# Kernel optimization log

Hardware: AMD Instinct MI355X
Metric: run time of the kernel (lower is better)

The kernel has to match this reference:

```python
import jax, jax.numpy as jnp
import numpy as np
from jax import lax

H = 512   # hidden_size
O = 256   # output_size
B = 64    # batch
S = 1024  # encoder sequence length
T = 256   # decoder timesteps


def setup_inputs() -> dict:
    key = jax.random.key(0)
    ks = jax.random.split(key, 10)
    bound = 1.0 / np.sqrt(H)  # PyTorch LSTM/Linear init scale
    return {
        "encoder_outputs": jax.random.normal(ks[0], (B, S, H), jnp.float32),
        "hidden": jax.random.normal(ks[1], (1, B, H), jnp.float32),
        "cell": jax.random.normal(ks[2], (1, B, H), jnp.float32),
        "target": jax.random.normal(ks[3], (B, T, O), jnp.float32),
        # LSTM params (gate order i, f, g, o as in PyTorch)
        "W_ih": jax.random.uniform(ks[4], (4 * H, H + O), jnp.float32, -bound, bound),
        "W_hh": jax.random.uniform(ks[5], (4 * H, H), jnp.float32, -bound, bound),
        "b_ih": jax.random.uniform(ks[6], (4 * H,), jnp.float32, -bound, bound),
        "b_hh": jax.random.uniform(ks[7], (4 * H,), jnp.float32, -bound, bound),
        # FC params
        "W_fc": jax.random.uniform(ks[8], (O, H), jnp.float32, -bound, bound),
        "b_fc": jax.random.uniform(ks[9], (O,), jnp.float32, -bound, bound),
    }


def reference(encoder_outputs, hidden, cell, target, W_ih, W_hh, b_ih, b_hh, W_fc, b_fc):
    h0 = hidden[0]  # [B, H]
    c0 = cell[0]    # [B, H]

    def step(carry, x_t):
        h, c = carry
        # Attention: dot-product scores over encoder positions
        scores = jnp.einsum("bsh,bh->bs", encoder_outputs, h)      # [B, S]
        attn = jax.nn.softmax(scores, axis=1)
        context = jnp.einsum("bs,bsh->bh", attn, encoder_outputs)  # [B, H]
        x = jnp.concatenate([context, x_t], axis=-1)               # [B, H+O]
        # Single-step LSTM cell (PyTorch gate order i, f, g, o)
        gates = x @ W_ih.T + b_ih + h @ W_hh.T + b_hh              # [B, 4H]
        i_g, f_g, g_g, o_g = jnp.split(gates, 4, axis=-1)
        i_g = jax.nn.sigmoid(i_g)
        f_g = jax.nn.sigmoid(f_g)
        g_g = jnp.tanh(g_g)
        o_g = jax.nn.sigmoid(o_g)
        c_new = f_g * c + i_g * g_g
        h_new = o_g * jnp.tanh(c_new)
        out = h_new @ W_fc.T + b_fc                                # [B, O]
        return (h_new, c_new), out

    _, outs = lax.scan(step, (h0, c0), jnp.swapaxes(target, 0, 1))  # outs: [T, B, O]
    return jnp.swapaxes(outs, 0, 1)  # [B, T, O]
```

## Files before the change

kernel.cpp:

```cpp
#include <hip/hip_runtime.h>

#define HH 512
#define OO 256
#define BB 64
#define SS 1024
#define TT 256
#define KK 1280

typedef __attribute__((ext_vector_type(8))) short bh8;
typedef __attribute__((ext_vector_type(8))) _Float16 hf8;
typedef __attribute__((ext_vector_type(4))) float fx4;

__device__ __forceinline__ unsigned short f2bf(float x) {
    union { float f; unsigned int u; } v; v.f = x;
    unsigned int r = v.u + 0x7fffu + ((v.u >> 16) & 1u);
    return (unsigned short)(r >> 16);
}
__device__ __forceinline__ float bf2f(unsigned short s) {
    union { unsigned int u; float f; } z; z.u = ((unsigned int)s) << 16; return z.f;
}

__global__ void prep_weights(const float* __restrict__ W_ih,
                             const float* __restrict__ W_hh,
                             unsigned short* __restrict__ wfH,
                             unsigned short* __restrict__ wfL) {
    int g = blockIdx.x * 256 + threadIdx.x;
    if (g >= 64 * 40 * 2 * 64) return;
    int lane = g & 63;
    int nt = (g >> 6) & 1;
    int kk = (g >> 7) % 40;
    int ht = (g >> 7) / 40;
    int c = nt * 16 + (lane & 15);
    int gate = c >> 3, rr = c & 7;
    int j = gate * 512 + ht * 8 + rr;
    int kbase = kk * 32 + (lane >> 4) * 8;
    unsigned short* dh = wfH + (size_t)g * 8;
    unsigned short* dl = wfL + (size_t)g * 8;
#pragma unroll
    for (int r = 0; r < 8; ++r) {
        int k = kbase + r;
        float v = (k < 768) ? W_ih[(size_t)j * 768 + k]
                            : W_hh[(size_t)j * 512 + (k - 768)];
        unsigned short hi = f2bf(v);
        dh[r] = hi;
        dl[r] = f2bf(v - bf2f(hi));
    }
}

__global__ void prep_misc(const float* __restrict__ hidden,
                          const float* __restrict__ cell,
                          float* __restrict__ h, float* __restrict__ c) {
    const int total = 32768 + 32768;
    for (int i = blockIdx.x * 256 + threadIdx.x; i < total; i += gridDim.x * 256) {
        if (i < 32768) h[i] = hidden[i];
        else           c[i - 32768] = cell[i - 32768];
    }
}

__global__ void prep_enc(const float* __restrict__ enc,
                         _Float16* __restrict__ ench) {
    const size_t i = ((size_t)blockIdx.x * 256 + threadIdx.x) * 8;
    const float4 a = *(const float4*)(enc + i);
    const float4 b = *(const float4*)(enc + i + 4);
    hf8 o;
    o[0] = (_Float16)a.x; o[1] = (_Float16)a.y;
    o[2] = (_Float16)a.z; o[3] = (_Float16)a.w;
    o[4] = (_Float16)b.x; o[5] = (_Float16)b.y;
    o[6] = (_Float16)b.z; o[7] = (_Float16)b.w;
    *(hf8*)(ench + i) = o;
}

__device__ __forceinline__ void fc_unit(int v, int tprev,
                                        const float* __restrict__ h,
                                        const float* __restrict__ W_fc,
                                        const float* __restrict__ b_fc,
                                        float* __restrict__ out,
                                        float (*shacc)[64]) {
    const int tid = threadIdx.x;
    const int b = v >> 2, oq = v & 3;
    const int ol = tid & 63, kq = tid >> 6;
    const int o = oq * 64 + ol;
    float acc = 0.f;
    const float* hp = h + b * HH + kq * 128;
    const float* wp = W_fc + (size_t)o * HH + kq * 128;
#pragma unroll 8
    for (int k2 = 0; k2 < 128; ++k2) acc += hp[k2] * wp[k2];
    shacc[kq][ol] = acc;
    __syncthreads();
    if (tid < 64) {
        float vv = shacc[0][tid] + shacc[1][tid]
                 + shacc[2][tid] + shacc[3][tid] + b_fc[oq * 64 + tid];
        out[((size_t)b * TT + tprev) * OO + oq * 64 + tid] = vv;
    }
}

template <int ENCF16>
__global__ void __launch_bounds__(256)
step_attnp(int t, const float* __restrict__ enc,
           const _Float16* __restrict__ ench,
           const float* __restrict__ h,
           float* __restrict__ pm, float* __restrict__ pl,
           float* __restrict__ pctx,
           const float* __restrict__ W_fc, const float* __restrict__ b_fc,
           float* __restrict__ out) {
    const int tid = threadIdx.x;
    const int lane = tid & 63;
    const int w = tid >> 6;

    __shared__ union {
        struct { float m[4]; float l[4]; float ctx[4][512]; } a;
        struct { float acc[4][64]; } o;
    } sh;

    const int u = blockIdx.x;
    if (u < 1024) {
        const int b = u >> 4, ch = u & 15;
        float m = -3.0e38f, l = 0.f;
        if (ENCF16) {
            const float* hb = h + b * HH + lane * 8;
            const float4 h0 = *(const float4*)hb;
            const float4 h1 = *(const float4*)(hb + 4);
            float cx[8];
#pragma unroll
            for (int j = 0; j < 8; ++j) cx[j] = 0.f;
            const _Float16* er =
                ench + ((size_t)(b * SS + ch * 64 + w * 16)) * HH + lane * 8;
            for (int rp = 0; rp < 8; ++rp) {
                const hf8 ev = *(const hf8*)er;
                const hf8 fv = *(const hf8*)(er + HH);
                float e[8], f[8];
#pragma unroll
                for (int j = 0; j < 8; ++j) {
                    e[j] = (float)ev[j];
                    f[j] = (float)fv[j];
                }
                float dA = e[0]*h0.x + e[1]*h0.y + e[2]*h0.z + e[3]*h0.w
                         + e[4]*h1.x + e[5]*h1.y + e[6]*h1.z + e[7]*h1.w;
                float dB = f[0]*h0.x + f[1]*h0.y + f[2]*h0.z + f[3]*h0.w
                         + f[4]*h1.x + f[5]*h1.y + f[6]*h1.z + f[7]*h1.w;
#pragma unroll
                for (int off = 32; off; off >>= 1) {
                    dA += __shfl_xor(dA, off);
                    dB += __shfl_xor(dB, off);
                }
                const float mx = fmaxf(dA, dB);
                if (mx > m) {
                    const float fs = __expf(m - mx);
                    l *= fs;
#pragma unroll
                    for (int j = 0; j < 8; ++j) cx[j] *= fs;
                    m = mx;
                }
                const float pA = __expf(dA - m);
                const float pB = __expf(dB - m);
                l += pA + pB;
#pragma unroll
                for (int j = 0; j < 8; ++j) cx[j] += pA * e[j] + pB * f[j];
                er += 2 * HH;
            }
            if (lane == 0) { sh.a.m[w] = m; sh.a.l[w] = l; }
            *(float4*)&sh.a.ctx[w][lane * 8]     = make_float4(cx[0], cx[1], cx[2], cx[3]);
            *(float4*)&sh.a.ctx[w][lane * 8 + 4] = make_float4(cx[4], cx[5], cx[6], cx[7]);
        } else {
            const float4 h0 = *(const float4*)(h + b * HH + lane * 4);
            const float4 h1 = *(const float4*)(h + b * HH + 256 + lane * 4);
            float4 c0 = {0, 0, 0, 0}, c1 = {0, 0, 0, 0};
            const float* er = enc + ((size_t)(b * SS + ch * 64 + w * 16)) * HH;
            for (int rp = 0; rp < 8; ++rp) {
                const float4 e0 = *(const float4*)(er + lane * 4);
                const float4 e1 = *(const float4*)(er + 256 + lane * 4);
                const float4 f0 = *(const float4*)(er + HH + lane * 4);
                const float4 f1 = *(const float4*)(er + HH + 256 + lane * 4);
                float dA = e0.x * h0.x + e0.y * h0.y + e0.z * h0.z + e0.w * h0.w
                         + e1.x * h1.x + e1.y * h1.y + e1.z * h1.z + e1.w * h1.w;
                float dB = f0.x * h0.x + f0.y * h0.y + f0.z * h0.z + f0.w * h0.w
                         + f1.x * h1.x + f1.y * h1.y + f1.z * h1.z + f1.w * h1.w;
#pragma unroll
                for (int off = 32; off; off >>= 1) {
                    dA += __shfl_xor(dA, off);
                    dB += __shfl_xor(dB, off);
                }
                const float mx = fmaxf(dA, dB);
                if (mx > m) {
                    const float fs = __expf(m - mx);
                    l *= fs;
                    c0.x *= fs; c0.y *= fs; c0.z *= fs; c0.w *= fs;
                    c1.x *= fs; c1.y *= fs; c1.z *= fs; c1.w *= fs;
                    m = mx;
                }
                const float pA = __expf(dA - m);
                const float pB = __expf(dB - m);
                l += pA + pB;
                c0.x += pA * e0.x + pB * f0.x; c0.y += pA * e0.y + pB * f0.y;
                c0.z += pA * e0.z + pB * f0.z; c0.w += pA * e0.w + pB * f0.w;
                c1.x += pA * e1.x + pB * f1.x; c1.y += pA * e1.y + pB * f1.y;
                c1.z += pA * e1.z + pB * f1.z; c1.w += pA * e1.w + pB * f1.w;
                er += 2 * HH;
            }
            if (lane == 0) { sh.a.m[w] = m; sh.a.l[w] = l; }
            *(float4*)&sh.a.ctx[w][lane * 4] = c0;
            *(float4*)&sh.a.ctx[w][256 + lane * 4] = c1;
        }
        __syncthreads();
        float M = fmaxf(fmaxf(sh.a.m[0], sh.a.m[1]), fmaxf(sh.a.m[2], sh.a.m[3]));
        float wg[4]; float ls = 0.f;
#pragma unroll
        for (int q = 0; q < 4; ++q) { wg[q] = __expf(sh.a.m[q] - M); ls += wg[q] * sh.a.l[q]; }
        const int hh = tid * 2;
        float v0 = wg[0] * sh.a.ctx[0][hh] + wg[1] * sh.a.ctx[1][hh]
                 + wg[2] * sh.a.ctx[2][hh] + wg[3] * sh.a.ctx[3][hh];
        float v1 = wg[0] * sh.a.ctx[0][hh + 1] + wg[1] * sh.a.ctx[1][hh + 1]
                 + wg[2] * sh.a.ctx[2][hh + 1] + wg[3] * sh.a.ctx[3][hh + 1];
        float* pc = pctx + ((size_t)(b * 16 + ch)) * HH;
        *(float2*)(pc + hh) = make_float2(v0, v1);
        if (tid == 0) { pm[b * 16 + ch] = M; pl[b * 16 + ch] = ls; }
    } else if (t > 0) {
        fc_unit(u - 1024, t - 1, h, W_fc, b_fc, out, sh.o.acc);
    }
}

__global__ void __launch_bounds__(256)
step_combine(int t, const float* __restrict__ target, const float* __restrict__ h,
             const float* __restrict__ pm, const float* __restrict__ pl,
             const float* __restrict__ pctx,
             unsigned short* __restrict__ xbh, unsigned short* __restrict__ xbl) {
    const int tid = threadIdx.x;
    const int b = blockIdx.x;
    float Mb = -3.0e38f;
#pragma unroll
    for (int q2 = 0; q2 < 16; ++q2) Mb = fmaxf(Mb, pm[b * 16 + q2]);
    float wq[16]; float lsb = 0.f;
#pragma unroll
    for (int q2 = 0; q2 < 16; ++q2) {
        wq[q2] = __expf(pm[b * 16 + q2] - Mb);
        lsb += wq[q2] * pl[b * 16 + q2];
    }
    const float inv = 1.0f / lsb;
    const int h2 = tid * 2;
    float s0 = 0.f, s1 = 0.f;
#pragma unroll
    for (int q2 = 0; q2 < 16; ++q2) {
        const float* pc2 = pctx + ((size_t)(b * 16 + q2)) * HH + h2;
        s0 += wq[q2] * pc2[0];
        s1 += wq[q2] * pc2[1];
    }
    s0 *= inv; s1 *= inv;
    unsigned short a0 = f2bf(s0), a1 = f2bf(s1);
    xbh[b * KK + h2]     = a0;  xbl[b * KK + h2]     = f2bf(s0 - bf2f(a0));
    xbh[b * KK + h2 + 1] = a1;  xbl[b * KK + h2 + 1] = f2bf(s1 - bf2f(a1));
    if (tid < 128) {
        const float* tg = target + ((size_t)b * TT + t) * OO + tid * 2;
        unsigned short t0 = f2bf(tg[0]), t1 = f2bf(tg[1]);
        xbh[b * KK + 512 + tid * 2]     = t0;
        xbh[b * KK + 512 + tid * 2 + 1] = t1;
        xbl[b * KK + 512 + tid * 2]     = f2bf(tg[0] - bf2f(t0));
        xbl[b * KK + 512 + tid * 2 + 1] = f2bf(tg[1] - bf2f(t1));
    }
    const float hv0 = h[b * HH + h2], hv1 = h[b * HH + h2 + 1];
    unsigned short g0 = f2bf(hv0), g1 = f2bf(hv1);
    xbh[b * KK + 768 + h2]     = g0;  xbl[b * KK + 768 + h2]     = f2bf(hv0 - bf2f(g0));
    xbh[b * KK + 768 + h2 + 1] = g1;  xbl[b * KK + 768 + h2 + 1] = f2bf(hv1 - bf2f(g1));
}

__global__ void __launch_bounds__(256)
step_gates(const unsigned short* __restrict__ xbh,
           const unsigned short* __restrict__ xbl,
           const unsigned short* __restrict__ wfH,
           const unsigned short* __restrict__ wfL,
           const float* __restrict__ b_ih, const float* __restrict__ b_hh,
           float* __restrict__ h, float* __restrict__ c) {
    const int tid = threadIdx.x;
    const int lane = tid & 63;
    const int w = tid >> 6;
    __shared__ float g[64][32];

    const int ht = blockIdx.x;
    fx4 a0 = {0, 0, 0, 0}, a1 = {0, 0, 0, 0};
    const int bro = 16 * w + (lane & 15);
    const int kg = lane >> 4;
    const size_t wbase = (size_t)ht * 40 * 2 * 512;
    for (int kk = 0; kk < 40; ++kk) {
        const size_t aoff = (size_t)bro * KK + kk * 32 + kg * 8;
        bh8 avh = *(const bh8*)(xbh + aoff);
        bh8 avl = *(const bh8*)(xbl + aoff);
        bh8 b0h = *(const bh8*)(wfH + wbase + (kk * 2 + 0) * 512 + lane * 8);
        bh8 b1h = *(const bh8*)(wfH + wbase + (kk * 2 + 1) * 512 + lane * 8);
        bh8 b0l = *(const bh8*)(wfL + wbase + (kk * 2 + 0) * 512 + lane * 8);
        bh8 b1l = *(const bh8*)(wfL + wbase + (kk * 2 + 1) * 512 + lane * 8);
        a0 = __builtin_amdgcn_mfma_f32_16x16x32_bf16(avh, b0h, a0, 0, 0, 0);
        a0 = __builtin_amdgcn_mfma_f32_16x16x32_bf16(avl, b0h, a0, 0, 0, 0);
        a0 = __builtin_amdgcn_mfma_f32_16x16x32_bf16(avh, b0l, a0, 0, 0, 0);
        a1 = __builtin_amdgcn_mfma_f32_16x16x32_bf16(avh, b1h, a1, 0, 0, 0);
        a1 = __builtin_amdgcn_mfma_f32_16x16x32_bf16(avl, b1h, a1, 0, 0, 0);
        a1 = __builtin_amdgcn_mfma_f32_16x16x32_bf16(avh, b1l, a1, 0, 0, 0);
    }
    const int crow = (lane >> 4) * 4;
#pragma unroll
    for (int r = 0; r < 4; ++r) {
        g[16 * w + crow + r][lane & 15]        = a0[r];
        g[16 * w + crow + r][16 + (lane & 15)] = a1[r];
    }
    __syncthreads();
#pragma unroll
    for (int p = 0; p < 2; ++p) {
        const int idx = tid * 2 + p;
        const int b = idx >> 3, r = idx & 7;
        const int hidx = ht * 8 + r;
        float gi = g[b][r]      + b_ih[hidx]        + b_hh[hidx];
        float gf = g[b][8 + r]  + b_ih[512 + hidx]  + b_hh[512 + hidx];
        float gg = g[b][16 + r] + b_ih[1024 + hidx] + b_hh[1024 + hidx];
        float go = g[b][24 + r] + b_ih[1536 + hidx] + b_hh[1536 + hidx];
        float ig = 1.f / (1.f + __expf(-gi));
        float fg = 1.f / (1.f + __expf(-gf));
        float g2 = tanhf(gg);
        float og = 1.f / (1.f + __expf(-go));
        float cn = fg * c[b * HH + hidx] + ig * g2;
        float hn = og * tanhf(cn);
        c[b * HH + hidx] = cn;
        h[b * HH + hidx] = hn;
    }
}

__global__ void __launch_bounds__(256)
fc_final(const float* __restrict__ h, const float* __restrict__ W_fc,
         const float* __restrict__ b_fc, float* __restrict__ out) {
    __shared__ float acc[4][64];
    fc_unit(blockIdx.x, TT - 1, h, W_fc, b_fc, out, acc);
}

extern "C" void kernel_launch(void* const* d_in, const int* in_sizes, int n_in,
                              void* d_out, int out_size, void* d_ws, size_t ws_size,
                              hipStream_t stream) {
    const float* enc    = (const float*)d_in[0];
    const float* hidden = (const float*)d_in[1];
    const float* cellp  = (const float*)d_in[2];
    const float* target = (const float*)d_in[3];
    const float* W_ih   = (const float*)d_in[4];
    const float* W_hh   = (const float*)d_in[5];
    const float* b_ih   = (const float*)d_in[6];
    const float* b_hh   = (const float*)d_in[7];
    const float* W_fc   = (const float*)d_in[8];
    const float* b_fc   = (const float*)d_in[9];
    float* out = (float*)d_out;

    char* base = (char*)d_ws;
    float* h              = (float*)(base + 0);
    float* c              = (float*)(base + 131072);
    unsigned short* wfH   = (unsigned short*)(base + 262144);
    unsigned short* wfL   = (unsigned short*)(base + 5505024);
    unsigned short* xbh   = (unsigned short*)(base + 10747904);
    unsigned short* xbl   = (unsigned short*)(base + 10911744);
    float* pm             = (float*)(base + 11075584);
    float* pl             = (float*)(base + 11079680);
    float* pctx           = (float*)(base + 11083776);
    _Float16* ench        = (_Float16*)(base + 13180928);
    const size_t NEED_H = 13180928ULL + 67108864ULL;

    const bool use_ench = (ws_size >= NEED_H);

    prep_weights<<<dim3(1280), dim3(256), 0, stream>>>(W_ih, W_hh, wfH, wfL);
    prep_misc<<<dim3(256), dim3(256), 0, stream>>>(hidden, cellp, h, c);
    if (use_ench)
        prep_enc<<<dim3(16384), dim3(256), 0, stream>>>(enc, ench);

    for (int t = 0; t < TT; ++t) {
        if (use_ench)
            step_attnp<1><<<dim3(1280), dim3(256), 0, stream>>>(
                t, enc, ench, h, pm, pl, pctx, W_fc, b_fc, out);
        else
            step_attnp<0><<<dim3(1280), dim3(256), 0, stream>>>(
                t, enc, ench, h, pm, pl, pctx, W_fc, b_fc, out);
        step_combine<<<dim3(64), dim3(256), 0, stream>>>(
            t, target, h, pm, pl, pctx, xbh, xbl);
        step_gates<<<dim3(64), dim3(256), 0, stream>>>(
            xbh, xbl, wfH, wfL, b_ih, b_hh, h, c);
    }
    fc_final<<<dim3(256), dim3(256), 0, stream>>>(h, W_fc, b_fc, out);
}
```

Measured before the change: 10.53 ms.

## Use fp16 for FC weights and partial contexts, unroll attention by four

Converts W_fc to fp16 once in the prep kernel and reads it in the per-step FC, and stores the per-chunk attention context partials as fp16 instead of fp32. The attention loop now processes four encoder rows per iteration with a single online-softmax rescale, which gives more loads in flight and fewer max/rescale branches. The fp32 encoder fallback is removed and the fp16 encoder copy is made unconditional, even though the workspace size is no longer checked. These changes cut memory traffic and instruction overhead in the recurrent loop, at the cost of lower precision in the FC weights and context partials.

```diff
diff --git a/kernel.cpp b/kernel.cpp
--- a/kernel.cpp
+++ b/kernel.cpp
@@ -10,20 +10,21 @@
 typedef __attribute__((ext_vector_type(8))) short bh8;
 typedef __attribute__((ext_vector_type(8))) _Float16 hf8;
 typedef __attribute__((ext_vector_type(4))) float fx4;
-
-__device__ __forceinline__ unsigned short f2bf(float x) {
+typedef unsigned short ushort_t;
+
+__device__ __forceinline__ ushort_t f2bf(float x) {
     union { float f; unsigned int u; } v; v.f = x;
     unsigned int r = v.u + 0x7fffu + ((v.u >> 16) & 1u);
-    return (unsigned short)(r >> 16);
-}
-__device__ __forceinline__ float bf2f(unsigned short s) {
+    return (ushort_t)(r >> 16);
+}
+__device__ __forceinline__ float bf2f(ushort_t s) {
     union { unsigned int u; float f; } z; z.u = ((unsigned int)s) << 16; return z.f;
 }
 
 __global__ void prep_weights(const float* __restrict__ W_ih,
                              const float* __restrict__ W_hh,
-                             unsigned short* __restrict__ wfH,
-                             unsigned short* __restrict__ wfL) {
+                             ushort_t* __restrict__ wfH,
+                             ushort_t* __restrict__ wfL) {
     int g = blockIdx.x * 256 + threadIdx.x;
     if (g >= 64 * 40 * 2 * 64) return;
     int lane = g & 63;
@@ -34,14 +35,14 @@
     int gate = c >> 3, rr = c & 7;
     int j = gate * 512 + ht * 8 + rr;
     int kbase = kk * 32 + (lane >> 4) * 8;
-    unsigned short* dh = wfH + (size_t)g * 8;
-    unsigned short* dl = wfL + (size_t)g * 8;
+    ushort_t* dh = wfH + (size_t)g * 8;
+    ushort_t* dl = wfL + (size_t)g * 8;
 #pragma unroll
     for (int r = 0; r < 8; ++r) {
         int k = kbase + r;
         float v = (k < 768) ? W_ih[(size_t)j * 768 + k]
                             : W_hh[(size_t)j * 512 + (k - 768)];
-        unsigned short hi = f2bf(v);
+        ushort_t hi = f2bf(v);
         dh[r] = hi;
         dl[r] = f2bf(v - bf2f(hi));
     }
@@ -49,16 +50,19 @@
 
 __global__ void prep_misc(const float* __restrict__ hidden,
                           const float* __restrict__ cell,
-                          float* __restrict__ h, float* __restrict__ c) {
-    const int total = 32768 + 32768;
+                          const float* __restrict__ W_fc,
+                          float* __restrict__ h, float* __restrict__ c,
+                          _Float16* __restrict__ wfc16) {
+    const int total = 32768 + 32768 + 131072;
     for (int i = blockIdx.x * 256 + threadIdx.x; i < total; i += gridDim.x * 256) {
-        if (i < 32768) h[i] = hidden[i];
-        else           c[i - 32768] = cell[i - 32768];
-    }
-}
-
-__global__ void prep_enc(const float* __restrict__ enc,
-                         _Float16* __restrict__ ench) {
+        if (i < 32768)       h[i] = hidden[i];
+        else if (i < 65536)  c[i - 32768] = cell[i - 32768];
+        else                 wfc16[i - 65536] = (_Float16)W_fc[i - 65536];
+    }
+}
+
+__global__ void prep_ench(const float* __restrict__ enc,
+                          _Float16* __restrict__ ench) {
     const size_t i = ((size_t)blockIdx.x * 256 + threadIdx.x) * 8;
     const float4 a = *(const float4*)(enc + i);
     const float4 b = *(const float4*)(enc + i + 4);
@@ -72,7 +76,7 @@
 
 __device__ __forceinline__ void fc_unit(int v, int tprev,
                                         const float* __restrict__ h,
-                                        const float* __restrict__ W_fc,
+                                        const _Float16* __restrict__ wfc16,
                                         const float* __restrict__ b_fc,
                                         float* __restrict__ out,
                                         float (*shacc)[64]) {
@@ -82,9 +86,9 @@
     const int o = oq * 64 + ol;
     float acc = 0.f;
     const float* hp = h + b * HH + kq * 128;
-    const float* wp = W_fc + (size_t)o * HH + kq * 128;
+    const _Float16* wp = wfc16 + (size_t)o * HH + kq * 128;
 #pragma unroll 8
-    for (int k2 = 0; k2 < 128; ++k2) acc += hp[k2] * wp[k2];
+    for (int k2 = 0; k2 < 128; ++k2) acc += hp[k2] * (float)wp[k2];
     shacc[kq][ol] = acc;
     __syncthreads();
     if (tid < 64) {
@@ -94,14 +98,12 @@
     }
 }
 
-template <int ENCF16>
 __global__ void __launch_bounds__(256)
-step_attnp(int t, const float* __restrict__ enc,
-           const _Float16* __restrict__ ench,
+step_attnp(int t, const _Float16* __restrict__ ench,
            const float* __restrict__ h,
            float* __restrict__ pm, float* __restrict__ pl,
-           float* __restrict__ pctx,
-           const float* __restrict__ W_fc, const float* __restrict__ b_fc,
+           _Float16* __restrict__ pctx,
+           const _Float16* __restrict__ wfc16, const float* __restrict__ b_fc,
            float* __restrict__ out) {
     const int tid = threadIdx.x;
     const int lane = tid & 63;
@@ -116,91 +118,61 @@
     if (u < 1024) {
         const int b = u >> 4, ch = u & 15;
         float m = -3.0e38f, l = 0.f;
-        if (ENCF16) {
-            const float* hb = h + b * HH + lane * 8;
-            const float4 h0 = *(const float4*)hb;
-            const float4 h1 = *(const float4*)(hb + 4);
-            float cx[8];
-#pragma unroll
-            for (int j = 0; j < 8; ++j) cx[j] = 0.f;
-            const _Float16* er =
-                ench + ((size_t)(b * SS + ch * 64 + w * 16)) * HH + lane * 8;
-            for (int rp = 0; rp < 8; ++rp) {
-                const hf8 ev = *(const hf8*)er;
-                const hf8 fv = *(const hf8*)(er + HH);
-                float e[8], f[8];
-#pragma unroll
-                for (int j = 0; j < 8; ++j) {
-                    e[j] = (float)ev[j];
-                    f[j] = (float)fv[j];
-                }
-                float dA = e[0]*h0.x + e[1]*h0.y + e[2]*h0.z + e[3]*h0.w
-                         + e[4]*h1.x + e[5]*h1.y + e[6]*h1.z + e[7]*h1.w;
-                float dB = f[0]*h0.x + f[1]*h0.y + f[2]*h0.z + f[3]*h0.w
-                         + f[4]*h1.x + f[5]*h1.y + f[6]*h1.z + f[7]*h1.w;
-#pragma unroll
-                for (int off = 32; off; off >>= 1) {
-                    dA += __shfl_xor(dA, off);
-                    dB += __shfl_xor(dB, off);
-                }
-                const float mx = fmaxf(dA, dB);
-                if (mx > m) {
-                    const float fs = __expf(m - mx);
-                    l *= fs;
-#pragma unroll
-                    for (int j = 0; j < 8; ++j) cx[j] *= fs;
-                    m = mx;
-                }
-                const float pA = __expf(dA - m);
-                const float pB = __expf(dB - m);
-                l += pA + pB;
-#pragma unroll
-                for (int j = 0; j < 8; ++j) cx[j] += pA * e[j] + pB * f[j];
-                er += 2 * HH;
+        const float* hb = h + b * HH + lane * 8;
+        const float4 h0 = *(const float4*)hb;
+        const float4 h1 = *(const float4*)(hb + 4);
+        float cx[8];
+#pragma unroll
+        for (int j = 0; j < 8; ++j) cx[j] = 0.f;
+        const _Float16* er =
+            ench + ((size_t)(b * SS + ch * 64 + w * 16)) * HH + lane * 8;
+        for (int g4 = 0; g4 < 4; ++g4) {
+            const hf8 v0 = *(const hf8*)er;
+            const hf8 v1 = *(const hf8*)(er + HH);
+            const hf8 v2 = *(const hf8*)(er + 2 * HH);
+            const hf8 v3 = *(const hf8*)(er + 3 * HH);
+            float e0[8], e1[8], e2[8], e3[8];
+#pragma unroll
+            for (int j = 0; j < 8; ++j) {
+                e0[j] = (float)v0[j]; e1[j] = (float)v1[j];
+                e2[j] = (float)v2[j]; e3[j] = (float)v3[j];
             }
-            if (lane == 0) { sh.a.m[w] = m; sh.a.l[w] = l; }
-            *(float4*)&sh.a.ctx[w][lane * 8]     = make_float4(cx[0], cx[1], cx[2], cx[3]);
-            *(float4*)&sh.a.ctx[w][lane * 8 + 4] = make_float4(cx[4], cx[5], cx[6], cx[7]);
-        } else {
-            const float4 h0 = *(const float4*)(h + b * HH + lane * 4);
-            const float4 h1 = *(const float4*)(h + b * HH + 256 + lane * 4);
-            float4 c0 = {0, 0, 0, 0}, c1 = {0, 0, 0, 0};
-            const float* er = enc + ((size_t)(b * SS + ch * 64 + w * 16)) * HH;
-            for (int rp = 0; rp < 8; ++rp) {
-                const float4 e0 = *(const float4*)(er + lane * 4);
-                const float4 e1 = *(const float4*)(er + 256 + lane * 4);
-                const float4 f0 = *(const float4*)(er + HH + lane * 4);
-                const float4 f1 = *(const float4*)(er + HH + 256 + lane * 4);
-                float dA = e0.x * h0.x + e0.y * h0.y + e0.z * h0.z + e0.w * h0.w
-                         + e1.x * h1.x + e1.y * h1.y + e1.z * h1.z + e1.w * h1.w;
-                float dB = f0.x * h0.x + f0.y * h0.y + f0.z * h0.z + f0.w * h0.w
-                         + f1.x * h1.x + f1.y * h1.y + f1.z * h1.z + f1.w * h1.w;
-#pragma unroll
-                for (int off = 32; off; off >>= 1) {
-                    dA += __shfl_xor(dA, off);
-                    dB += __shfl_xor(dB, off);
-                }
-                const float mx = fmaxf(dA, dB);
-                if (mx > m) {
-                    const float fs = __expf(m - mx);
-                    l *= fs;
-                    c0.x *= fs; c0.y *= fs; c0.z *= fs; c0.w *= fs;
-                    c1.x *= fs; c1.y *= fs; c1.z *= fs; c1.w *= fs;
-                    m = mx;
-                }
-                const float pA = __expf(dA - m);
-                const float pB = __expf(dB - m);
-                l += pA + pB;
-                c0.x += pA * e0.x + pB * f0.x; c0.y += pA * e0.y + pB * f0.y;
-                c0.z += pA * e0.z + pB * f0.z; c0.w += pA * e0.w + pB * f0.w;
-                c1.x += pA * e1.x + pB * f1.x; c1.y += pA * e1.y + pB * f1.y;
-                c1.z += pA * e1.z + pB * f1.z; c1.w += pA * e1.w + pB * f1.w;
-                er += 2 * HH;
+            float d0 = e0[0]*h0.x + e0[1]*h0.y + e0[2]*h0.z + e0[3]*h0.w
+                     + e0[4]*h1.x + e0[5]*h1.y + e0[6]*h1.z + e0[7]*h1.w;
+            float d1 = e1[0]*h0.x + e1[1]*h0.y + e1[2]*h0.z + e1[3]*h0.w
+                     + e1[4]*h1.x + e1[5]*h1.y + e1[6]*h1.z + e1[7]*h1.w;
+            float d2 = e2[0]*h0.x + e2[1]*h0.y + e2[2]*h0.z + e2[3]*h0.w
+                     + e2[4]*h1.x + e2[5]*h1.y + e2[6]*h1.z + e2[7]*h1.w;
+            float d3 = e3[0]*h0.x + e3[1]*h0.y + e3[2]*h0.z + e3[3]*h0.w
+                     + e3[4]*h1.x + e3[5]*h1.y + e3[6]*h1.z + e3[7]*h1.w;
+#pragma unroll
+            for (int off = 32; off; off >>= 1) {
+                d0 += __shfl_xor(d0, off);
+                d1 += __shfl_xor(d1, off);
+                d2 += __shfl_xor(d2, off);
+                d3 += __shfl_xor(d3, off);
             }
-            if (lane == 0) { sh.a.m[w] = m; sh.a.l[w] = l; }
-            *(float4*)&sh.a.ctx[w][lane * 4] = c0;
-            *(float4*)&sh.a.ctx[w][256 + lane * 4] = c1;
+            const float mx = fmaxf(fmaxf(d0, d1), fmaxf(d2, d3));
+            if (mx > m) {
+                const float fs = __expf(m - mx);
+                l *= fs;
+#pragma unroll
+                for (int j = 0; j < 8; ++j) cx[j] *= fs;
+                m = mx;
+            }
+            const float p0 = __expf(d0 - m);
+            const float p1 = __expf(d1 - m);
+            const float p2 = __expf(d2 - m);
+            const float p3 = __expf(d3 - m);
+            l += (p0 + p1) + (p2 + p3);
+#pragma unroll
+            for (int j = 0; j < 8; ++j)
+                cx[j] += p0 * e0[j] + p1 * e1[j] + p2 * e2[j] + p3 * e3[j];
+            er += 4 * HH;
         }
+        if (lane == 0) { sh.a.m[w] = m; sh.a.l[w] = l; }
+        *(float4*)&sh.a.ctx[w][lane * 8]     = make_float4(cx[0], cx[1], cx[2], cx[3]);
+        *(float4*)&sh.a.ctx[w][lane * 8 + 4] = make_float4(cx[4], cx[5], cx[6], cx[7]);
         __syncthreads();
         float M = fmaxf(fmaxf(sh.a.m[0], sh.a.m[1]), fmaxf(sh.a.m[2], sh.a.m[3]));
         float wg[4]; float ls = 0.f;
@@ -211,19 +183,20 @@
                  + wg[2] * sh.a.ctx[2][hh] + wg[3] * sh.a.ctx[3][hh];
         float v1 = wg[0] * sh.a.ctx[0][hh + 1] + wg[1] * sh.a.ctx[1][hh + 1]
                  + wg[2] * sh.a.ctx[2][hh + 1] + wg[3] * sh.a.ctx[3][hh + 1];
-        float* pc = pctx + ((size_t)(b * 16 + ch)) * HH;
-        *(float2*)(pc + hh) = make_float2(v0, v1);
+        _Float16* pc = pctx + ((size_t)(b * 16 + ch)) * HH;
+        pc[hh]     = (_Float16)v0;
+        pc[hh + 1] = (_Float16)v1;
         if (tid == 0) { pm[b * 16 + ch] = M; pl[b * 16 + ch] = ls; }
     } else if (t > 0) {
-        fc_unit(u - 1024, t - 1, h, W_fc, b_fc, out, sh.o.acc);
+        fc_unit(u - 1024, t - 1, h, wfc16, b_fc, out, sh.o.acc);
     }
 }
 
 __global__ void __launch_bounds__(256)
 step_combine(int t, const float* __restrict__ target, const float* __restrict__ h,
              const float* __restrict__ pm, const float* __restrict__ pl,
-             const float* __restrict__ pctx,
-             unsigned short* __restrict__ xbh, unsigned short* __restrict__ xbl) {
+             const _Float16* __restrict__ pctx,
+             ushort_t* __restrict__ xbh, ushort_t* __restrict__ xbl) {
     const int tid = threadIdx.x;
     const int b = blockIdx.x;
     float Mb = -3.0e38f;
@@ -240,33 +213,33 @@
     float s0 = 0.f, s1 = 0.f;
 #pragma unroll
     for (int q2 = 0; q2 < 16; ++q2) {
-        const float* pc2 = pctx + ((size_t)(b * 16 + q2)) * HH + h2;
-        s0 += wq[q2] * pc2[0];
-        s1 += wq[q2] * pc2[1];
+        const _Float16* pc2 = pctx + ((size_t)(b * 16 + q2)) * HH + h2;
+        s0 += wq[q2] * (float)pc2[0];
+        s1 += wq[q2] * (float)pc2[1];
     }
     s0 *= inv; s1 *= inv;
-    unsigned short a0 = f2bf(s0), a1 = f2bf(s1);
+    ushort_t a0 = f2bf(s0), a1 = f2bf(s1);
     xbh[b * KK + h2]     = a0;  xbl[b * KK + h2]     = f2bf(s0 - bf2f(a0));
     xbh[b * KK + h2 + 1] = a1;  xbl[b * KK + h2 + 1] = f2bf(s1 - bf2f(a1));
     if (tid < 128) {
         const float* tg = target + ((size_t)b * TT + t) * OO + tid * 2;
-        unsigned short t0 = f2bf(tg[0]), t1 = f2bf(tg[1]);
+        ushort_t t0 = f2bf(tg[0]), t1 = f2bf(tg[1]);
         xbh[b * KK + 512 + tid * 2]     = t0;
         xbh[b * KK + 512 + tid * 2 + 1] = t1;
         xbl[b * KK + 512 + tid * 2]     = f2bf(tg[0] - bf2f(t0));
         xbl[b * KK + 512 + tid * 2 + 1] = f2bf(tg[1] - bf2f(t1));
     }
     const float hv0 = h[b * HH + h2], hv1 = h[b * HH + h2 + 1];
-    unsigned short g0 = f2bf(hv0), g1 = f2bf(hv1);
+    ushort_t g0 = f2bf(hv0), g1 = f2bf(hv1);
     xbh[b * KK + 768 + h2]     = g0;  xbl[b * KK + 768 + h2]     = f2bf(hv0 - bf2f(g0));
     xbh[b * KK + 768 + h2 + 1] = g1;  xbl[b * KK + 768 + h2 + 1] = f2bf(hv1 - bf2f(g1));
 }
 
 __global__ void __launch_bounds__(256)
-step_gates(const unsigned short* __restrict__ xbh,
-           const unsigned short* __restrict__ xbl,
-           const unsigned short* __restrict__ wfH,
-           const unsigned short* __restrict__ wfL,
+step_gates(const ushort_t* __restrict__ xbh,
+           const ushort_t* __restrict__ xbl,
+           const ushort_t* __restrict__ wfH,
+           const ushort_t* __restrict__ wfL,
            const float* __restrict__ b_ih, const float* __restrict__ b_hh,
            float* __restrict__ h, float* __restrict__ c) {
     const int tid = threadIdx.x;
@@ -322,10 +295,10 @@
 }
 
 __global__ void __launch_bounds__(256)
-fc_final(const float* __restrict__ h, const float* __restrict__ W_fc,
+fc_final(const float* __restrict__ h, const _Float16* __restrict__ wfc16,
          const float* __restrict__ b_fc, float* __restrict__ out) {
     __shared__ float acc[4][64];
-    fc_unit(blockIdx.x, TT - 1, h, W_fc, b_fc, out, acc);
+    fc_unit(blockIdx.x, TT - 1, h, wfc16, b_fc, out, acc);
 }
 
 extern "C" void kernel_launch(void* const* d_in, const int* in_sizes, int n_in,
@@ -344,36 +317,29 @@
     float* out = (float*)d_out;
 
     char* base = (char*)d_ws;
-    float* h              = (float*)(base + 0);
-    float* c              = (float*)(base + 131072);
-    unsigned short* wfH   = (unsigned short*)(base + 262144);
-    unsigned short* wfL   = (unsigned short*)(base + 5505024);
-    unsigned short* xbh   = (unsigned short*)(base + 10747904);
-    unsigned short* xbl   = (unsigned short*)(base + 10911744);
-    float* pm             = (float*)(base + 11075584);
-    float* pl             = (float*)(base + 11079680);
-    float* pctx           = (float*)(base + 11083776);
-    _Float16* ench        = (_Float16*)(base + 13180928);
-    const size_t NEED_H = 13180928ULL + 67108864ULL;
-
-    const bool use_ench = (ws_size >= NEED_H);
+    float* h            = (float*)(base + 0);
+    float* c            = (float*)(base + 131072);
+    ushort_t* wfH       = (ushort_t*)(base + 262144);
+    ushort_t* wfL       = (ushort_t*)(base + 5505024);
+    ushort_t* xbh       = (ushort_t*)(base + 10747904);
+    ushort_t* xbl       = (ushort_t*)(base + 10911744);
+    float* pm           = (float*)(base + 11075584);
+    float* pl           = (float*)(base + 11079680);
+    _Float16* wfc16     = (_Float16*)(base + 11083776);
+    _Float16* pctx      = (_Float16*)(base + 11345920);
+    _Float16* ench      = (_Float16*)(base + 12394496);
 
     prep_weights<<<dim3(1280), dim3(256), 0, stream>>>(W_ih, W_hh, wfH, wfL);
-    prep_misc<<<dim3(256), dim3(256), 0, stream>>>(hidden, cellp, h, c);
-    if (use_ench)
-        prep_enc<<<dim3(16384), dim3(256), 0, stream>>>(enc, ench);
+    prep_misc<<<dim3(768), dim3(256), 0, stream>>>(hidden, cellp, W_fc, h, c, wfc16);
+    prep_ench<<<dim3(16384), dim3(256), 0, stream>>>(enc, ench);
 
     for (int t = 0; t < TT; ++t) {
-        if (use_ench)
-            step_attnp<1><<<dim3(1280), dim3(256), 0, stream>>>(
-                t, enc, ench, h, pm, pl, pctx, W_fc, b_fc, out);
-        else
-            step_attnp<0><<<dim3(1280), dim3(256), 0, stream>>>(
-                t, enc, ench, h, pm, pl, pctx, W_fc, b_fc, out);
+        step_attnp<<<dim3(1280), dim3(256), 0, stream>>>(
+            t, ench, h, pm, pl, pctx, wfc16, b_fc, out);
         step_combine<<<dim3(64), dim3(256), 0, stream>>>(
             t, target, h, pm, pl, pctx, xbh, xbl);
         step_gates<<<dim3(64), dim3(256), 0, stream>>>(
             xbh, xbl, wfH, wfL, b_ih, b_hh, h, c);
     }
-    fc_final<<<dim3(256), dim3(256), 0, stream>>>(h, W_fc, b_fc, out);
-}
+    fc_final<<<dim3(256), dim3(256), 0, stream>>>(h, wfc16, b_fc, out);
+}
```

Result: no change. 10.65 ms (+1.2%).
